# Kernel optimization log

Measured on AMD Instinct MI355X. Metric: run time of the kernel, lower is better.

Reference implementation:

```python
import jax, jax.numpy as jnp
import numpy as np

FEA_DIM = 256
NUM_HEADS = 8
B, N = 32, 48


def setup_inputs() -> dict:
    key = jax.random.key(0)
    ks = jax.random.split(key, 30)
    d = FEA_DIM
    inp = {
        "async_fea": jax.random.normal(ks[0], (B, N, d), dtype=jnp.float32),
        "sync_fea": jax.random.normal(ks[1], (B, N, d), dtype=jnp.float32),
        "async_adj": jax.random.randint(ks[2], (B, N, N), 0, 2, dtype=jnp.int32),
        "sync_adj": jax.random.randint(ks[3], (B, N, N), 0, 2, dtype=jnp.int32),
    }
    i = 4
    for pref in ("a_", "s_"):
        for nm in ("Wq", "Wk", "Wv", "Wo", "Wm"):
            inp[pref + nm] = 0.02 * jax.random.normal(ks[i], (d, d), dtype=jnp.float32); i += 1
            inp[pref + nm.replace("W", "b")] = 0.02 * jax.random.normal(ks[i], (d,), dtype=jnp.float32); i += 1
    return inp


def _aggregate(x_src, adj, fallback, Wq, bq, Wk, bk, Wv, bv, Wo, bo, Wm, bm):
    """For each target t: self-attention among neighbor set {s : adj[b,s,t] > 0}
    of x_src, mean-pool over neighbors, divide by count again, linear map.
    Targets with no neighbors fall back to `fallback`."""
    Bb, Nn, D = x_src.shape
    H = NUM_HEADS
    dh = D // H
    q = (x_src @ Wq.T + bq).reshape(Bb, Nn, H, dh)
    k = (x_src @ Wk.T + bk).reshape(Bb, Nn, H, dh)
    v = (x_src @ Wv.T + bv).reshape(Bb, Nn, H, dh)
    # shared pairwise scores among source nodes: [B, H, Q, K]
    scores = jnp.einsum("bqhd,bkhd->bhqk", q, k) / jnp.sqrt(jnp.float32(dh))
    # neighbor mask per target: adj[b, s, t] > 0 -> m[b, t, s]
    m = jnp.transpose(adj > 0, (0, 2, 1))  # [B, T, S] bool
    # per-target masked softmax over keys: logits [B, T, H, Q, K]
    key_bias = jnp.where(m[:, :, None, None, :], 0.0, -1e9)
    attn = jax.nn.softmax(scores[:, None] + key_bias, axis=-1)  # [B,T,H,Q,K]
    out = jnp.einsum("bthqk,bkhd->bthqd", attn, v).reshape(Bb, Nn, Nn, D)  # [B,T,Q,D]
    out = out @ Wo.T + bo
    mf = m.astype(out.dtype)  # [B, T, Q]
    cnt = mf.sum(-1)  # [B, T]
    denom = jnp.maximum(cnt, 1.0)
    # torch: mean over valid queries, then / edge_cnt  => sum / cnt^2
    pooled = jnp.einsum("btq,btqd->btd", mf, out) / (denom * denom)[..., None]
    mapped = pooled @ Wm.T + bm
    return jnp.where((cnt > 0)[..., None], mapped, fallback)


def reference(async_fea, sync_fea, async_adj, sync_adj,
              a_Wq, a_bq, a_Wk, a_bk, a_Wv, a_bv, a_Wo, a_bo, a_Wm, a_bm,
              s_Wq, s_bq, s_Wk, s_bk, s_Wv, s_bv, s_Wo, s_bo, s_Wm, s_bm):
    refined_async = _aggregate(sync_fea, sync_adj, async_fea,
                               a_Wq, a_bq, a_Wk, a_bk, a_Wv, a_bv, a_Wo, a_bo, a_Wm, a_bm)
    refined_sync = _aggregate(async_fea, async_adj, sync_fea,
                              s_Wq, s_bq, s_Wk, s_bk, s_Wv, s_bv, s_Wo, s_bo, s_Wm, s_bm)
    return jnp.concatenate([refined_async, refined_sync, async_fea, sync_fea], axis=2)
```

## Files before the change

### kernel.cpp

```cpp
#include <hip/hip_runtime.h>

typedef __attribute__((ext_vector_type(8))) short short8v;
typedef __attribute__((ext_vector_type(4))) float f32x4;
typedef unsigned short u16t;

#define XP 264
#define SP 52

#define E_OFF    0
#define ET_OFF   39936
#define QB_OFF   79872
#define KB_OFF   105216
#define VT_OFF   130560
#define MSK_OFF  157184
#define CNT_OFF  158848
#define SM_SIZE  158912
#define XB_OFF   E_OFF
#define IV_OFF   QB_OFF
#define PL_OFF   (QB_OFF + 13312)
#define YV_OFF   KB_OFF
#define PO_OFF   (KB_OFF + 13312)

__device__ __forceinline__ u16t f2bf(float f) {
    union { float f; unsigned u; } v; v.f = f;
    unsigned u = v.u;
    return (u16t)((u + 0x7FFFu + ((u >> 16) & 1u)) >> 16);
}
__device__ __forceinline__ float bf2f(u16t u) {
    union { unsigned u; float f; } v; v.u = ((unsigned)u) << 16; return v.f;
}
__device__ __forceinline__ short8v cvt8(const float* p) {
    float4 lo = *(const float4*)p;
    float4 hi = *(const float4*)(p + 4);
    union { uint4 u; short8v s; } r;
    asm("v_cvt_pk_bf16_f32 %0, %1, %2" : "=v"(r.u.x) : "v"(lo.x), "v"(lo.y));
    asm("v_cvt_pk_bf16_f32 %0, %1, %2" : "=v"(r.u.y) : "v"(lo.z), "v"(lo.w));
    asm("v_cvt_pk_bf16_f32 %0, %1, %2" : "=v"(r.u.z) : "v"(hi.x), "v"(hi.y));
    asm("v_cvt_pk_bf16_f32 %0, %1, %2" : "=v"(r.u.w) : "v"(hi.z), "v"(hi.w));
    return r.s;
}
__device__ __forceinline__ short8v ld52(const u16t* p) {
    union { uint2 u[2]; short8v s; } r;
    r.u[0] = *(const uint2*)(p);
    r.u[1] = *(const uint2*)(p + 4);
    return r.s;
}

struct AggParams {
    const float *async_fea, *sync_fea;
    const int *async_adj, *sync_adj;
    const float *aWq, *abq, *aWk, *abk, *aWv, *abv, *aWo, *abo, *aWm, *abm;
    const float *sWq, *sbq, *sWk, *sbk, *sWv, *sbv, *sWo, *sbo, *sWm, *sbm;
    float *out;
};

__global__ __launch_bounds__(512) void block_kernel(AggParams p)
{
    __shared__ __attribute__((aligned(16))) char sm[SM_SIZE];
    u16t* E_   = (u16t*)(sm + E_OFF);
    u16t* ET_  = (u16t*)(sm + ET_OFF);
    u16t* Xb   = (u16t*)(sm + XB_OFF);
    u16t* Qb   = (u16t*)(sm + QB_OFF);
    u16t* Kb   = (u16t*)(sm + KB_OFF);
    u16t* VT   = (u16t*)(sm + VT_OFF);
    u16t* mskb = (u16t*)(sm + MSK_OFF);
    u16t* iv_  = (u16t*)(sm + IV_OFF);
    u16t* yv_  = (u16t*)(sm + YV_OFF);
    u16t* P_l  = (u16t*)(sm + PL_OFF);
    u16t* po_  = (u16t*)(sm + PO_OFF);
    float* cnt_l = (float*)(sm + CNT_OFF);

    const int bid = blockIdx.x, tid = threadIdx.x;
    const int agg = bid >> 7, rem = bid & 127;
    const int b = rem >> 2, tg = rem & 3;
    const int wave = tid >> 6, lane = tid & 63;
    const int l15 = lane & 15, g = lane >> 4;
    const int row_base = b * 48 + tg * 12;

    const float* Xsrc = agg ? p.async_fea : p.sync_fea;
    const float* fb   = agg ? p.sync_fea  : p.async_fea;
    const int*   adj  = agg ? p.async_adj : p.sync_adj;

    #pragma unroll
    for (int l = 0; l < 3; ++l) {
        int idx = l * 4096 + tid * 8;
        int row = idx >> 8, col = idx & 255;
        *(short8v*)(Xb + row * XP + col) = cvt8(Xsrc + (b * 48 + row) * 256 + col);
    }
    for (int e = tid; e < 16 * SP; e += 512) {
        int tt = e / SP, k = e - tt * SP;
        u16t v = 0;
        if (tt < 12 && k < 48)
            v = (adj[(b * 48 + k) * 48 + tg * 12 + tt] > 0) ? (u16t)0x3F80 : (u16t)0;
        mskb[e] = v;
    }
    {
        const float4* fb4 = (const float4*)fb;
        float4* out4 = (float4*)p.out;
        for (int e = tid; e < 768; e += 512) {
            int r = e >> 6, c = e & 63;
            out4[(row_base + r) * 256 + 128 + agg * 64 + c] =
                fb4[(row_base + r) * 64 + c];
        }
    }
    __syncthreads();
    if (tid < 12) {
        float c = 0.f;
        for (int s = 0; s < 48; ++s) c += bf2f(mskb[tid * SP + s]);
        cnt_l[tid] = c;
    }

    {
        const float *Wq, *Wk, *Wv, *bq, *bk, *bv;
        if (agg == 0) { Wq = p.aWq; Wk = p.aWk; Wv = p.aWv; bq = p.abq; bk = p.abk; bv = p.abv; }
        else          { Wq = p.sWq; Wk = p.sWk; Wv = p.sWv; bq = p.sbq; bk = p.sbk; bv = p.sbv; }
        for (int cmi = wave; cmi < 16; cmi += 8) {
            int cm = cmi * 16;
            const float* Wqp = Wq + (cm + l15) * 256 + g * 8;
            const float* Wkp = Wk + (cm + l15) * 256 + g * 8;
            const float* Wvp = Wv + (cm + l15) * 256 + g * 8;
            short8v bqf[8], bkf[8], bvf[8];
            #pragma unroll
            for (int kk = 0; kk < 8; ++kk) {
                bqf[kk] = cvt8(Wqp + kk * 32);
                bkf[kk] = cvt8(Wkp + kk * 32);
                bvf[kk] = cvt8(Wvp + kk * 32);
            }
            f32x4 aq[3], ak[3], av[3];
            #pragma unroll
            for (int rt = 0; rt < 3; ++rt) {
                f32x4 z = {0.f, 0.f, 0.f, 0.f};
                aq[rt] = z; ak[rt] = z; av[rt] = z;
            }
            #pragma unroll
            for (int rt = 0; rt < 3; ++rt)
                #pragma unroll
                for (int kk = 0; kk < 8; ++kk) {
                    short8v a = *(const short8v*)(Xb + (rt * 16 + l15) * XP + kk * 32 + g * 8);
                    aq[rt] = __builtin_amdgcn_mfma_f32_16x16x32_bf16(a, bqf[kk], aq[rt], 0, 0, 0);
                    ak[rt] = __builtin_amdgcn_mfma_f32_16x16x32_bf16(a, bkf[kk], ak[rt], 0, 0, 0);
                    av[rt] = __builtin_amdgcn_mfma_f32_16x16x32_bf16(a, bvf[kk], av[rt], 0, 0, 0);
                }
            float bqv = bq[cm + l15], bkv = bk[cm + l15], bvv = bv[cm + l15];
            #pragma unroll
            for (int rt = 0; rt < 3; ++rt)
                #pragma unroll
                for (int i = 0; i < 4; ++i) {
                    int row = rt * 16 + g * 4 + i;
                    Qb[row * XP + cm + l15] = f2bf(aq[rt][i] + bqv);
                    Kb[row * XP + cm + l15] = f2bf(ak[rt][i] + bkv);
                    VT[(cm + l15) * SP + row] = f2bf(av[rt][i] + bvv);
                }
        }
    }
    __syncthreads();

    const float scale = 0.17677669529663687f;
    #pragma unroll
    for (int jj = 0; jj < 3; ++jj) {
        int job = wave * 3 + jj;
        int h = job / 3, qt = job % 3;
        short8v a = *(const short8v*)(Qb + (qt * 16 + l15) * XP + h * 32 + g * 8);
        f32x4 acc[3];
        #pragma unroll
        for (int kt = 0; kt < 3; ++kt) {
            short8v kb = *(const short8v*)(Kb + (kt * 16 + l15) * XP + h * 32 + g * 8);
            f32x4 z = {0.f, 0.f, 0.f, 0.f};
            acc[kt] = __builtin_amdgcn_mfma_f32_16x16x32_bf16(a, kb, z, 0, 0, 0);
        }
        float sc[3][4], rm[4];
        #pragma unroll
        for (int i = 0; i < 4; ++i) {
            #pragma unroll
            for (int kt = 0; kt < 3; ++kt) sc[kt][i] = acc[kt][i] * scale;
            rm[i] = fmaxf(fmaxf(sc[0][i], sc[1][i]), sc[2][i]);
        }
        #pragma unroll
        for (int m = 1; m <= 8; m <<= 1)
            #pragma unroll
            for (int i = 0; i < 4; ++i) rm[i] = fmaxf(rm[i], __shfl_xor(rm[i], m));
        #pragma unroll
        for (int kt = 0; kt < 3; ++kt)
            #pragma unroll
            for (int i = 0; i < 4; ++i) {
                u16t ev = f2bf(__expf(sc[kt][i] - rm[i]));
                int q = qt * 16 + g * 4 + i, k = kt * 16 + l15;
                E_[(h * 48 + q) * SP + k] = ev;
                ET_[(h * 48 + k) * SP + q] = ev;
            }
    }
    __syncthreads();

    #pragma unroll
    for (int jj = 0; jj < 3; ++jj) {
        int rt = wave * 3 + jj;
        const u16t* Arow = E_ + (rt * 16 + l15) * SP;
        const u16t* Brow = mskb + l15 * SP;
        f32x4 acc = {0.f, 0.f, 0.f, 0.f};
        short8v a0 = ld52(Arow + g * 8), b0 = ld52(Brow + g * 8);
        acc = __builtin_amdgcn_mfma_f32_16x16x32_bf16(a0, b0, acc, 0, 0, 0);
        short8v a1 = {0,0,0,0,0,0,0,0}, b1 = {0,0,0,0,0,0,0,0};
        if (g < 2) { a1 = ld52(Arow + 32 + g * 8); b1 = ld52(Brow + 32 + g * 8); }
        acc = __builtin_amdgcn_mfma_f32_16x16x32_bf16(a1, b1, acc, 0, 0, 0);
        #pragma unroll
        for (int i = 0; i < 4; ++i) {
            int row = rt * 16 + g * 4 + i;
            int h = row / 48, q = row - h * 48;
            float mq = bf2f(mskb[l15 * SP + q]);
            float ivv = (mq > 0.f) ? (1.f / acc[i]) : 0.f;
            iv_[(h * 16 + l15) * SP + q] = f2bf(ivv);
        }
    }
    __syncthreads();

    #pragma unroll
    for (int jj = 0; jj < 3; ++jj) {
        int job = wave * 3 + jj;
        int h = job / 3, kt = job % 3;
        const u16t* Arow = iv_ + (h * 16 + l15) * SP;
        const u16t* Brow = ET_ + (h * 48 + kt * 16 + l15) * SP;
        f32x4 acc = {0.f, 0.f, 0.f, 0.f};
        short8v a0 = ld52(Arow + g * 8), b0 = ld52(Brow + g * 8);
        acc = __builtin_amdgcn_mfma_f32_16x16x32_bf16(a0, b0, acc, 0, 0, 0);
        short8v a1 = {0,0,0,0,0,0,0,0}, b1 = {0,0,0,0,0,0,0,0};
        if (g < 2) { a1 = ld52(Arow + 32 + g * 8); b1 = ld52(Brow + 32 + g * 8); }
        acc = __builtin_amdgcn_mfma_f32_16x16x32_bf16(a1, b1, acc, 0, 0, 0);
        #pragma unroll
        for (int i = 0; i < 4; ++i) {
            int tt = g * 4 + i, k = kt * 16 + l15;
            float mk = bf2f(mskb[tt * SP + k]);
            yv_[(h * 16 + tt) * SP + k] = f2bf(acc[i] * mk);
        }
    }
    __syncthreads();

    #pragma unroll
    for (int jj = 0; jj < 2; ++jj) {
        int job = wave * 2 + jj;
        int h = job >> 1, dt = job & 1;
        const u16t* Arow = yv_ + (h * 16 + l15) * SP;
        const u16t* Brow = VT + (h * 32 + dt * 16 + l15) * SP;
        f32x4 acc = {0.f, 0.f, 0.f, 0.f};
        short8v a0 = ld52(Arow + g * 8), b0 = ld52(Brow + g * 8);
        acc = __builtin_amdgcn_mfma_f32_16x16x32_bf16(a0, b0, acc, 0, 0, 0);
        short8v a1 = {0,0,0,0,0,0,0,0}, b1 = {0,0,0,0,0,0,0,0};
        if (g < 2) { a1 = ld52(Arow + 32 + g * 8); b1 = ld52(Brow + 32 + g * 8); }
        acc = __builtin_amdgcn_mfma_f32_16x16x32_bf16(a1, b1, acc, 0, 0, 0);
        #pragma unroll
        for (int i = 0; i < 4; ++i)
            P_l[(g * 4 + i) * XP + h * 32 + dt * 16 + l15] = f2bf(acc[i]);
    }
    __syncthreads();

    {
        const float* Wo = agg ? p.sWo : p.aWo;
        const float* bo = agg ? p.sbo : p.abo;
        #pragma unroll
        for (int jj = 0; jj < 2; ++jj) {
            int ct = wave * 2 + jj;
            f32x4 acc = {0.f, 0.f, 0.f, 0.f};
            const float* Wp = Wo + (ct * 16 + l15) * 256 + g * 8;
            #pragma unroll
            for (int kk = 0; kk < 8; ++kk) {
                short8v a = *(const short8v*)(P_l + l15 * XP + kk * 32 + g * 8);
                short8v bf = cvt8(Wp + kk * 32);
                acc = __builtin_amdgcn_mfma_f32_16x16x32_bf16(a, bf, acc, 0, 0, 0);
            }
            int c = ct * 16 + l15;
            float bov = bo[c];
            #pragma unroll
            for (int i = 0; i < 4; ++i) {
                int t = g * 4 + i;
                float val = 0.f;
                if (t < 12) {
                    float cn = cnt_l[t];
                    float i1 = (cn > 0.f) ? 1.f / cn : 0.f;
                    val = acc[i] * i1 * i1 + bov * i1;
                }
                po_[t * XP + c] = f2bf(val);
            }
        }
    }
    __syncthreads();

    {
        const float* Wm = agg ? p.sWm : p.aWm;
        const float* bm = agg ? p.sbm : p.abm;
        #pragma unroll
        for (int jj = 0; jj < 2; ++jj) {
            int ct = wave * 2 + jj;
            f32x4 acc = {0.f, 0.f, 0.f, 0.f};
            const float* Wp = Wm + (ct * 16 + l15) * 256 + g * 8;
            #pragma unroll
            for (int kk = 0; kk < 8; ++kk) {
                short8v a = *(const short8v*)(po_ + l15 * XP + kk * 32 + g * 8);
                short8v bf = cvt8(Wp + kk * 32);
                acc = __builtin_amdgcn_mfma_f32_16x16x32_bf16(a, bf, acc, 0, 0, 0);
            }
            int c = ct * 16 + l15;
            float bmv = bm[c];
            #pragma unroll
            for (int i = 0; i < 4; ++i) {
                int t = g * 4 + i;
                if (t < 12) {
                    int grow = row_base + t;
                    float cn = cnt_l[t];
                    float val = (cn > 0.f) ? (acc[i] + bmv) : fb[grow * 256 + c];
                    p.out[grow * 1024 + agg * 256 + c] = val;
                }
            }
        }
    }
}

extern "C" void kernel_launch(void* const* d_in, const int* in_sizes, int n_in,
                              void* d_out, int out_size, void* d_ws, size_t ws_size,
                              hipStream_t stream)
{
    AggParams p;
    p.async_fea = (const float*)d_in[0];
    p.sync_fea  = (const float*)d_in[1];
    p.async_adj = (const int*)d_in[2];
    p.sync_adj  = (const int*)d_in[3];
    p.aWq = (const float*)d_in[4];   p.abq = (const float*)d_in[5];
    p.aWk = (const float*)d_in[6];   p.abk = (const float*)d_in[7];
    p.aWv = (const float*)d_in[8];   p.abv = (const float*)d_in[9];
    p.aWo = (const float*)d_in[10];  p.abo = (const float*)d_in[11];
    p.aWm = (const float*)d_in[12];  p.abm = (const float*)d_in[13];
    p.sWq = (const float*)d_in[14];  p.sbq = (const float*)d_in[15];
    p.sWk = (const float*)d_in[16];  p.sbk = (const float*)d_in[17];
    p.sWv = (const float*)d_in[18];  p.sbv = (const float*)d_in[19];
    p.sWo = (const float*)d_in[20];  p.sbo = (const float*)d_in[21];
    p.sWm = (const float*)d_in[22];  p.sbm = (const float*)d_in[23];
    p.out = (float*)d_out;

    block_kernel<<<256, 512, 0, stream>>>(p);
}
```

Baseline: 53.05 us.

## Split fused aggregation kernel into weight-convert, QKV, scores and aggregation kernels

The single fused kernel recomputed the full QKV projection per target-group block, four times per batch, and converted weights to bf16 repeatedly. The work is now split into four launches: a one-shot bf16 weight conversion into workspace, a standalone QKV GEMM kernel across 576 blocks, a scores/exp kernel writing E and E^T to global memory, and a slimmer aggregation kernel that reads these buffers. This removes the redundant projection work and cuts shared memory for the final kernel. In exchange it adds launch overhead and global-memory round trips for the intermediates.

```diff
diff --git a/kernel.cpp b/kernel.cpp
--- a/kernel.cpp
+++ b/kernel.cpp
@@ -3,23 +3,6 @@
 typedef __attribute__((ext_vector_type(8))) short short8v;
 typedef __attribute__((ext_vector_type(4))) float f32x4;
 typedef unsigned short u16t;
-
-#define XP 264
-#define SP 52
-
-#define E_OFF    0
-#define ET_OFF   39936
-#define QB_OFF   79872
-#define KB_OFF   105216
-#define VT_OFF   130560
-#define MSK_OFF  157184
-#define CNT_OFF  158848
-#define SM_SIZE  158912
-#define XB_OFF   E_OFF
-#define IV_OFF   QB_OFF
-#define PL_OFF   (QB_OFF + 13312)
-#define YV_OFF   KB_OFF
-#define PO_OFF   (KB_OFF + 13312)
 
 __device__ __forceinline__ u16t f2bf(float f) {
     union { float f; unsigned u; } v; v.f = f;
@@ -46,28 +29,124 @@
     return r.s;
 }
 
-struct AggParams {
+struct Params {
     const float *async_fea, *sync_fea;
     const int *async_adj, *sync_adj;
-    const float *aWq, *abq, *aWk, *abk, *aWv, *abv, *aWo, *abo, *aWm, *abm;
-    const float *sWq, *sbq, *sWk, *sbk, *sWv, *sbv, *sWo, *sbo, *sWm, *sbm;
+    const float *Wf[10];
+    const float *bqkv[6];
+    const float *bo_[2], *bm_[2];
+    u16t *Wb;
+    u16t *Qb, *Kb, *Vb;
+    u16t *Eg, *ETg;
     float *out;
 };
 
-__global__ __launch_bounds__(512) void block_kernel(AggParams p)
-{
-    __shared__ __attribute__((aligned(16))) char sm[SM_SIZE];
-    u16t* E_   = (u16t*)(sm + E_OFF);
-    u16t* ET_  = (u16t*)(sm + ET_OFF);
-    u16t* Xb   = (u16t*)(sm + XB_OFF);
-    u16t* Qb   = (u16t*)(sm + QB_OFF);
-    u16t* Kb   = (u16t*)(sm + KB_OFF);
+__global__ __launch_bounds__(256) void convert_kernel(Params p)
+{
+    int g8 = (blockIdx.x * 256 + threadIdx.x) * 8;
+    int w = g8 >> 16;
+    int off = g8 & 65535;
+    *(short8v*)(p.Wb + g8) = cvt8(p.Wf[w] + off);
+}
+
+__global__ __launch_bounds__(256) void qkv_kernel(Params p)
+{
+    int bid = blockIdx.x;
+    int agg = bid / 288, rem = bid % 288;
+    int rt = rem / 12, ct = rem % 12;
+    int wave = threadIdx.x >> 6, lane = threadIdx.x & 63;
+    int l15 = lane & 15, g = lane >> 4;
+    int row0 = rt * 64 + wave * 16;
+    int mat = ct >> 2;
+    int cbase = (ct & 3) * 64;
+    const float* X = agg ? p.async_fea : p.sync_fea;
+    const float* Xp = X + (row0 + l15) * 256 + g * 8;
+    const u16t* Wp = p.Wb + (agg * 5 + mat) * 65536 + (cbase + l15) * 256 + g * 8;
+    f32x4 acc[4] = {{0,0,0,0},{0,0,0,0},{0,0,0,0},{0,0,0,0}};
+    #pragma unroll
+    for (int kk = 0; kk < 8; ++kk) {
+        short8v a = cvt8(Xp + kk * 32);
+        #pragma unroll
+        for (int j = 0; j < 4; ++j) {
+            short8v b = *(const short8v*)(Wp + j * 16 * 256 + kk * 32);
+            acc[j] = __builtin_amdgcn_mfma_f32_16x16x32_bf16(a, b, acc[j], 0, 0, 0);
+        }
+    }
+    const float* bias = p.bqkv[agg * 3 + mat];
+    u16t* dst = ((mat == 0) ? p.Qb : (mat == 1) ? p.Kb : p.Vb) + agg * 393216;
+    #pragma unroll
+    for (int j = 0; j < 4; ++j) {
+        int c = cbase + j * 16 + l15;
+        float bv = bias[c];
+        #pragma unroll
+        for (int i = 0; i < 4; ++i) {
+            int row = row0 + g * 4 + i;
+            dst[row * 256 + c] = f2bf(acc[j][i] + bv);
+        }
+    }
+}
+
+__global__ __launch_bounds__(192) void scores_kernel(Params p)
+{
+    int bid = blockIdx.x;
+    int agg = bid >> 8, r = bid & 255, b = r >> 3, h = r & 7;
+    int qt = threadIdx.x >> 6, lane = threadIdx.x & 63;
+    int l15 = lane & 15, g = lane >> 4;
+    const u16t* Qp = p.Qb + agg * 393216 + (b * 48 + qt * 16 + l15) * 256 + h * 32 + g * 8;
+    short8v a = *(const short8v*)Qp;
+    f32x4 acc[3];
+    #pragma unroll
+    for (int kt = 0; kt < 3; ++kt) {
+        const u16t* Kp = p.Kb + agg * 393216 + (b * 48 + kt * 16 + l15) * 256 + h * 32 + g * 8;
+        short8v kb = *(const short8v*)Kp;
+        f32x4 z = {0.f, 0.f, 0.f, 0.f};
+        acc[kt] = __builtin_amdgcn_mfma_f32_16x16x32_bf16(a, kb, z, 0, 0, 0);
+    }
+    const float scale = 0.17677669529663687f;
+    float sc[3][4], rm[4];
+    #pragma unroll
+    for (int i = 0; i < 4; ++i) {
+        #pragma unroll
+        for (int kt = 0; kt < 3; ++kt) sc[kt][i] = acc[kt][i] * scale;
+        rm[i] = fmaxf(fmaxf(sc[0][i], sc[1][i]), sc[2][i]);
+    }
+    #pragma unroll
+    for (int m = 1; m <= 8; m <<= 1)
+        #pragma unroll
+        for (int i = 0; i < 4; ++i) rm[i] = fmaxf(rm[i], __shfl_xor(rm[i], m));
+    u16t* Eb  = p.Eg  + (agg * 32 + b) * 18432 + h * 2304;
+    u16t* ETb = p.ETg + (agg * 32 + b) * 18432 + h * 2304;
+    #pragma unroll
+    for (int kt = 0; kt < 3; ++kt)
+        #pragma unroll
+        for (int i = 0; i < 4; ++i) {
+            u16t ev = f2bf(__expf(sc[kt][i] - rm[i]));
+            int q = qt * 16 + g * 4 + i, k = kt * 16 + l15;
+            Eb[q * 48 + k]  = ev;
+            ETb[k * 48 + q] = ev;
+        }
+}
+
+#define VT_OFF   0
+#define IV_OFF   26624
+#define YV_OFF   39936
+#define PL_OFF   53248
+#define PO_OFF   61696
+#define MSK_OFF  70144
+#define CNT_OFF  71808
+#define SM3_SIZE 71872
+#define SP 52
+#define XP 264
+
+__global__ __launch_bounds__(512) void agg_kernel(Params p)
+{
+    __shared__ __attribute__((aligned(16))) char sm[SM3_SIZE];
     u16t* VT   = (u16t*)(sm + VT_OFF);
-    u16t* mskb = (u16t*)(sm + MSK_OFF);
     u16t* iv_  = (u16t*)(sm + IV_OFF);
     u16t* yv_  = (u16t*)(sm + YV_OFF);
     u16t* P_l  = (u16t*)(sm + PL_OFF);
     u16t* po_  = (u16t*)(sm + PO_OFF);
+    u16t* mskb = (u16t*)(sm + MSK_OFF);
     float* cnt_l = (float*)(sm + CNT_OFF);
 
     const int bid = blockIdx.x, tid = threadIdx.x;
@@ -77,15 +156,19 @@
     const int l15 = lane & 15, g = lane >> 4;
     const int row_base = b * 48 + tg * 12;
 
-    const float* Xsrc = agg ? p.async_fea : p.sync_fea;
-    const float* fb   = agg ? p.sync_fea  : p.async_fea;
-    const int*   adj  = agg ? p.async_adj : p.sync_adj;
+    const float* fb  = agg ? p.sync_fea  : p.async_fea;
+    const int*   adj = agg ? p.async_adj : p.sync_adj;
+    const u16t* Egb  = p.Eg  + (agg * 32 + b) * 18432;
+    const u16t* ETb  = p.ETg + (agg * 32 + b) * 18432;
 
     #pragma unroll
     for (int l = 0; l < 3; ++l) {
         int idx = l * 4096 + tid * 8;
-        int row = idx >> 8, col = idx & 255;
-        *(short8v*)(Xb + row * XP + col) = cvt8(Xsrc + (b * 48 + row) * 256 + col);
+        int k = idx >> 8, d0 = idx & 255;
+        uint4 v = *(const uint4*)(p.Vb + agg * 393216 + (b * 48 + k) * 256 + d0);
+        const u16t* pv = (const u16t*)&v;
+        #pragma unroll
+        for (int j = 0; j < 8; ++j) VT[(d0 + j) * SP + k] = pv[j];
     }
     for (int e = tid; e < 16 * SP; e += 512) {
         int tt = e / SP, k = e - tt * SP;
@@ -110,97 +193,17 @@
         cnt_l[tid] = c;
     }
 
-    {
-        const float *Wq, *Wk, *Wv, *bq, *bk, *bv;
-        if (agg == 0) { Wq = p.aWq; Wk = p.aWk; Wv = p.aWv; bq = p.abq; bk = p.abk; bv = p.abv; }
-        else          { Wq = p.sWq; Wk = p.sWk; Wv = p.sWv; bq = p.sbq; bk = p.sbk; bv = p.sbv; }
-        for (int cmi = wave; cmi < 16; cmi += 8) {
-            int cm = cmi * 16;
-            const float* Wqp = Wq + (cm + l15) * 256 + g * 8;
-            const float* Wkp = Wk + (cm + l15) * 256 + g * 8;
-            const float* Wvp = Wv + (cm + l15) * 256 + g * 8;
-            short8v bqf[8], bkf[8], bvf[8];
-            #pragma unroll
-            for (int kk = 0; kk < 8; ++kk) {
-                bqf[kk] = cvt8(Wqp + kk * 32);
-                bkf[kk] = cvt8(Wkp + kk * 32);
-                bvf[kk] = cvt8(Wvp + kk * 32);
-            }
-            f32x4 aq[3], ak[3], av[3];
-            #pragma unroll
-            for (int rt = 0; rt < 3; ++rt) {
-                f32x4 z = {0.f, 0.f, 0.f, 0.f};
-                aq[rt] = z; ak[rt] = z; av[rt] = z;
-            }
-            #pragma unroll
-            for (int rt = 0; rt < 3; ++rt)
-                #pragma unroll
-                for (int kk = 0; kk < 8; ++kk) {
-                    short8v a = *(const short8v*)(Xb + (rt * 16 + l15) * XP + kk * 32 + g * 8);
-                    aq[rt] = __builtin_amdgcn_mfma_f32_16x16x32_bf16(a, bqf[kk], aq[rt], 0, 0, 0);
-                    ak[rt] = __builtin_amdgcn_mfma_f32_16x16x32_bf16(a, bkf[kk], ak[rt], 0, 0, 0);
-                    av[rt] = __builtin_amdgcn_mfma_f32_16x16x32_bf16(a, bvf[kk], av[rt], 0, 0, 0);
-                }
-            float bqv = bq[cm + l15], bkv = bk[cm + l15], bvv = bv[cm + l15];
-            #pragma unroll
-            for (int rt = 0; rt < 3; ++rt)
-                #pragma unroll
-                for (int i = 0; i < 4; ++i) {
-                    int row = rt * 16 + g * 4 + i;
-                    Qb[row * XP + cm + l15] = f2bf(aq[rt][i] + bqv);
-                    Kb[row * XP + cm + l15] = f2bf(ak[rt][i] + bkv);
-                    VT[(cm + l15) * SP + row] = f2bf(av[rt][i] + bvv);
-                }
-        }
-    }
-    __syncthreads();
-
-    const float scale = 0.17677669529663687f;
-    #pragma unroll
-    for (int jj = 0; jj < 3; ++jj) {
-        int job = wave * 3 + jj;
-        int h = job / 3, qt = job % 3;
-        short8v a = *(const short8v*)(Qb + (qt * 16 + l15) * XP + h * 32 + g * 8);
-        f32x4 acc[3];
-        #pragma unroll
-        for (int kt = 0; kt < 3; ++kt) {
-            short8v kb = *(const short8v*)(Kb + (kt * 16 + l15) * XP + h * 32 + g * 8);
-            f32x4 z = {0.f, 0.f, 0.f, 0.f};
-            acc[kt] = __builtin_amdgcn_mfma_f32_16x16x32_bf16(a, kb, z, 0, 0, 0);
-        }
-        float sc[3][4], rm[4];
-        #pragma unroll
-        for (int i = 0; i < 4; ++i) {
-            #pragma unroll
-            for (int kt = 0; kt < 3; ++kt) sc[kt][i] = acc[kt][i] * scale;
-            rm[i] = fmaxf(fmaxf(sc[0][i], sc[1][i]), sc[2][i]);
-        }
-        #pragma unroll
-        for (int m = 1; m <= 8; m <<= 1)
-            #pragma unroll
-            for (int i = 0; i < 4; ++i) rm[i] = fmaxf(rm[i], __shfl_xor(rm[i], m));
-        #pragma unroll
-        for (int kt = 0; kt < 3; ++kt)
-            #pragma unroll
-            for (int i = 0; i < 4; ++i) {
-                u16t ev = f2bf(__expf(sc[kt][i] - rm[i]));
-                int q = qt * 16 + g * 4 + i, k = kt * 16 + l15;
-                E_[(h * 48 + q) * SP + k] = ev;
-                ET_[(h * 48 + k) * SP + q] = ev;
-            }
-    }
-    __syncthreads();
-
     #pragma unroll
     for (int jj = 0; jj < 3; ++jj) {
         int rt = wave * 3 + jj;
-        const u16t* Arow = E_ + (rt * 16 + l15) * SP;
+        const u16t* Arow = Egb + (rt * 16 + l15) * 48;
         const u16t* Brow = mskb + l15 * SP;
         f32x4 acc = {0.f, 0.f, 0.f, 0.f};
-        short8v a0 = ld52(Arow + g * 8), b0 = ld52(Brow + g * 8);
+        short8v a0 = *(const short8v*)(Arow + g * 8);
+        short8v b0 = ld52(Brow + g * 8);
         acc = __builtin_amdgcn_mfma_f32_16x16x32_bf16(a0, b0, acc, 0, 0, 0);
         short8v a1 = {0,0,0,0,0,0,0,0}, b1 = {0,0,0,0,0,0,0,0};
-        if (g < 2) { a1 = ld52(Arow + 32 + g * 8); b1 = ld52(Brow + 32 + g * 8); }
+        if (g < 2) { a1 = *(const short8v*)(Arow + 32 + g * 8); b1 = ld52(Brow + 32 + g * 8); }
         acc = __builtin_amdgcn_mfma_f32_16x16x32_bf16(a1, b1, acc, 0, 0, 0);
         #pragma unroll
         for (int i = 0; i < 4; ++i) {
@@ -218,12 +221,13 @@
         int job = wave * 3 + jj;
         int h = job / 3, kt = job % 3;
         const u16t* Arow = iv_ + (h * 16 + l15) * SP;
-        const u16t* Brow = ET_ + (h * 48 + kt * 16 + l15) * SP;
+        const u16t* Brow = ETb + (h * 48 + kt * 16 + l15) * 48;
         f32x4 acc = {0.f, 0.f, 0.f, 0.f};
-        short8v a0 = ld52(Arow + g * 8), b0 = ld52(Brow + g * 8);
+        short8v a0 = ld52(Arow + g * 8);
+        short8v b0 = *(const short8v*)(Brow + g * 8);
         acc = __builtin_amdgcn_mfma_f32_16x16x32_bf16(a0, b0, acc, 0, 0, 0);
         short8v a1 = {0,0,0,0,0,0,0,0}, b1 = {0,0,0,0,0,0,0,0};
-        if (g < 2) { a1 = ld52(Arow + 32 + g * 8); b1 = ld52(Brow + 32 + g * 8); }
+        if (g < 2) { a1 = ld52(Arow + 32 + g * 8); b1 = *(const short8v*)(Brow + 32 + g * 8); }
         acc = __builtin_amdgcn_mfma_f32_16x16x32_bf16(a1, b1, acc, 0, 0, 0);
         #pragma unroll
         for (int i = 0; i < 4; ++i) {
@@ -253,17 +257,17 @@
     __syncthreads();
 
     {
-        const float* Wo = agg ? p.sWo : p.aWo;
-        const float* bo = agg ? p.sbo : p.abo;
+        const u16t* Wo = p.Wb + (agg * 5 + 3) * 65536;
+        const float* bo = p.bo_[agg];
         #pragma unroll
         for (int jj = 0; jj < 2; ++jj) {
             int ct = wave * 2 + jj;
             f32x4 acc = {0.f, 0.f, 0.f, 0.f};
-            const float* Wp = Wo + (ct * 16 + l15) * 256 + g * 8;
+            const u16t* Wp = Wo + (ct * 16 + l15) * 256 + g * 8;
             #pragma unroll
             for (int kk = 0; kk < 8; ++kk) {
                 short8v a = *(const short8v*)(P_l + l15 * XP + kk * 32 + g * 8);
-                short8v bf = cvt8(Wp + kk * 32);
+                short8v bf = *(const short8v*)(Wp + kk * 32);
                 acc = __builtin_amdgcn_mfma_f32_16x16x32_bf16(a, bf, acc, 0, 0, 0);
             }
             int c = ct * 16 + l15;
@@ -284,17 +288,17 @@
     __syncthreads();
 
     {
-        const float* Wm = agg ? p.sWm : p.aWm;
-        const float* bm = agg ? p.sbm : p.abm;
+        const u16t* Wm = p.Wb + (agg * 5 + 4) * 65536;
+        const float* bm = p.bm_[agg];
         #pragma unroll
         for (int jj = 0; jj < 2; ++jj) {
             int ct = wave * 2 + jj;
             f32x4 acc = {0.f, 0.f, 0.f, 0.f};
-            const float* Wp = Wm + (ct * 16 + l15) * 256 + g * 8;
+            const u16t* Wp = Wm + (ct * 16 + l15) * 256 + g * 8;
             #pragma unroll
             for (int kk = 0; kk < 8; ++kk) {
                 short8v a = *(const short8v*)(po_ + l15 * XP + kk * 32 + g * 8);
-                short8v bf = cvt8(Wp + kk * 32);
+                short8v bf = *(const short8v*)(Wp + kk * 32);
                 acc = __builtin_amdgcn_mfma_f32_16x16x32_bf16(a, bf, acc, 0, 0, 0);
             }
             int c = ct * 16 + l15;
@@ -317,22 +321,43 @@
                               void* d_out, int out_size, void* d_ws, size_t ws_size,
                               hipStream_t stream)
 {
-    AggParams p;
+    Params p;
     p.async_fea = (const float*)d_in[0];
     p.sync_fea  = (const float*)d_in[1];
     p.async_adj = (const int*)d_in[2];
     p.sync_adj  = (const int*)d_in[3];
-    p.aWq = (const float*)d_in[4];   p.abq = (const float*)d_in[5];
-    p.aWk = (const float*)d_in[6];   p.abk = (const float*)d_in[7];
-    p.aWv = (const float*)d_in[8];   p.abv = (const float*)d_in[9];
-    p.aWo = (const float*)d_in[10];  p.abo = (const float*)d_in[11];
-    p.aWm = (const float*)d_in[12];  p.abm = (const float*)d_in[13];
-    p.sWq = (const float*)d_in[14];  p.sbq = (const float*)d_in[15];
-    p.sWk = (const float*)d_in[16];  p.sbk = (const float*)d_in[17];
-    p.sWv = (const float*)d_in[18];  p.sbv = (const float*)d_in[19];
-    p.sWo = (const float*)d_in[20];  p.sbo = (const float*)d_in[21];
-    p.sWm = (const float*)d_in[22];  p.sbm = (const float*)d_in[23];
+    p.Wf[0] = (const float*)d_in[4];
+    p.Wf[1] = (const float*)d_in[6];
+    p.Wf[2] = (const float*)d_in[8];
+    p.Wf[3] = (const float*)d_in[10];
+    p.Wf[4] = (const float*)d_in[12];
+    p.Wf[5] = (const float*)d_in[14];
+    p.Wf[6] = (const float*)d_in[16];
+    p.Wf[7] = (const float*)d_in[18];
+    p.Wf[8] = (const float*)d_in[20];
+    p.Wf[9] = (const float*)d_in[22];
+    p.bqkv[0] = (const float*)d_in[5];
+    p.bqkv[1] = (const float*)d_in[7];
+    p.bqkv[2] = (const float*)d_in[9];
+    p.bqkv[3] = (const float*)d_in[15];
+    p.bqkv[4] = (const float*)d_in[17];
+    p.bqkv[5] = (const float*)d_in[19];
+    p.bo_[0] = (const float*)d_in[11];
+    p.bo_[1] = (const float*)d_in[21];
+    p.bm_[0] = (const float*)d_in[13];
+    p.bm_[1] = (const float*)d_in[23];
+
+    u16t* us = (u16t*)d_ws;
+    p.Wb  = us;
+    p.Qb  = p.Wb + 655360;
+    p.Kb  = p.Qb + 786432;
+    p.Vb  = p.Kb + 786432;
+    p.Eg  = p.Vb + 786432;
+    p.ETg = p.Eg + 1179648;
     p.out = (float*)d_out;
 
-    block_kernel<<<256, 512, 0, stream>>>(p);
-}
+    convert_kernel<<<320, 256, 0, stream>>>(p);
+    qkv_kernel<<<576, 256, 0, stream>>>(p);
+    scores_kernel<<<512, 192, 0, stream>>>(p);
+    agg_kernel<<<256, 512, 0, stream>>>(p);
+}
```

Result: no change. 52.98 us (-0.1%).
